# Performance work log

Measured on AMD Instinct MI355X. Metric: run time of the kernel, lower is better.

The kernel has to match this reference:

```python
import jax, jax.numpy as jnp
import numpy as np

# Dims: T time steps (PoissonEncoder seq_length=50), batch B, input N_IN, hidden H, labels L
T, B, N_IN, H, L = 50, 1024, 784, 256, 10
DT = 0.001            # norse default dt
TAU_SYN_INV = 100.0   # 1/0.01
TAU_MEM_INV = 50.0    # 1/0.02
V_LEAK, V_TH, V_RESET = 0.0, 0.5, 0.0
ALPHA = 100.0         # SuperSpike surrogate slope

@jax.custom_vjp
def superspike(x):
    # Heaviside forward, SuperSpike surrogate backward (norse 'super' method)
    return (x > 0).astype(x.dtype)

def _ss_fwd(x):
    return superspike(x), x

def _ss_bwd(x, g):
    return (g / (ALPHA * jnp.abs(x) + 1.0) ** 2,)

superspike.defvjp(_ss_fwd, _ss_bwd)

def setup_inputs() -> dict:
    key = jax.random.key(0)
    ks = jax.random.split(key, 5)
    # Poisson-encoded spike train, time-major [T, B, N_IN]
    x = (jax.random.uniform(ks[0], (T, B, N_IN)) < 0.3).astype(jnp.float32)
    Wi = jax.random.normal(ks[1], (H, N_IN), dtype=jnp.float32) / np.float32(np.sqrt(N_IN))
    Wr = jax.random.normal(ks[2], (H, H), dtype=jnp.float32) / np.float32(np.sqrt(H))
    Wout = jax.random.normal(ks[3], (L, H), dtype=jnp.float32) / np.float32(np.sqrt(H))
    bout = jnp.zeros((L,), dtype=jnp.float32)
    return {"x": x, "Wi": Wi, "Wr": Wr, "Wout": Wout, "bout": bout}

def reference(x, Wi, Wr, Wout, bout):
    Tw, Bb, _ = x.shape
    Hh = Wi.shape[0]
    Ll = Wout.shape[0]
    z0 = jnp.zeros((Bb, Hh), x.dtype)
    acc0 = jnp.zeros((Bb, Ll), x.dtype)

    def step(carry, x_t):
        z, v, i, acc = carry
        # LIF dynamics (norse lif_step)
        v_dec = v + DT * TAU_MEM_INV * ((V_LEAK - v) + i)   # voltage integration
        i_dec = i * (1.0 - DT * TAU_SYN_INV)                # synaptic current decay
        z_new = superspike(v_dec - V_TH)                    # spike
        v_new = (1.0 - z_new) * v_dec + z_new * V_RESET     # reset
        i_new = i_dec + x_t @ Wi.T + z @ Wr.T               # input + recurrent drive
        # per-step readout accumulation
        acc = acc + z_new @ Wout.T + bout
        return (z_new, v_new, i_new, acc), None

    (_, _, _, acc), _ = jax.lax.scan(step, (z0, z0, z0, acc0), x)
    return acc / Tw  # outputs.float() / time_window (is_test=False path)
```

## Files before the change

kernel.cpp:

```cpp
#include <hip/hip_runtime.h>
#include <cstdint>
#include <cstddef>

#define T_STEPS 50
#define B_SZ    1024
#define N_INP   784
#define H_SZ    256
#define L_SZ    10
#define M_TOT   (T_STEPS * B_SZ)
#define NK0     26
#define NSLICE  5

typedef int v4i  __attribute__((ext_vector_type(4)));
typedef int v16i __attribute__((ext_vector_type(16)));

__global__ __launch_bounds__(256) void transpose_wr(const float* __restrict__ Wr,
                                                    float* __restrict__ WrTz) {
    __shared__ float tile[32][33];
    int bx = blockIdx.x * 32, by = blockIdx.y * 32;
    int tx = threadIdx.x % 32, ty = threadIdx.x / 32;
    #pragma unroll
    for (int j = 0; j < 32; j += 8)
        tile[ty + j][tx] = Wr[(size_t)(by + ty + j) * H_SZ + bx + tx];
    __syncthreads();
    #pragma unroll
    for (int j = 0; j < 32; j += 8)
        WrTz[(size_t)(bx + ty + j) * H_SZ + by + tx] = tile[tx][ty + j];
}

__global__ __launch_bounds__(128) void prep_packed(const float* __restrict__ Wi,
                                                   uint8_t* __restrict__ SBp) {
    const int nt   = blockIdx.x;
    const int k0   = blockIdx.y * 2 + (threadIdx.x >> 6);
    const int lane = threadIdx.x & 63;
    const int h    = nt * 32 + (lane & 31);
    const int g    = k0 * 2 + (lane >> 5);

    int wd[NSLICE][4] = {};
    #pragma unroll
    for (int u = 0; u < 16; ++u) {
        double wv = 0.0;
        if (g < 49) wv = (double)Wi[(size_t)h * N_INP + g * 16 + u];
        double r = rint(wv * 0x1p40);
        #pragma unroll
        for (int j = 0; j < NSLICE - 1; ++j) {
            double q  = floor((r + 128.0) * 0.00390625);
            double dj = r - 256.0 * q;
            wd[j][u >> 2] |= ((int)dj & 0xFF) << ((u & 3) * 8);
            r = q;
        }
        wd[NSLICE - 1][u >> 2] |= ((int)r & 0xFF) << ((u & 3) * 8);
    }
    uint8_t* base = SBp + ((size_t)(nt * NK0 + k0) * NSLICE) * 1024 + lane * 16;
    #pragma unroll
    for (int j = 0; j < NSLICE; ++j)
        *(v4i*)(base + (size_t)j * 1024) = (v4i){wd[j][0], wd[j][1], wd[j][2], wd[j][3]};
}

__global__ __launch_bounds__(256) void pack_x(const float* __restrict__ X,
                                              uint8_t* __restrict__ Ap) {
    const int mt  = blockIdx.x;
    const int tid = threadIdx.x;
    #pragma unroll
    for (int i = 0; i < 7; ++i) {
        int s = tid + i * 256;
        if (s < NK0 * 64) {
            int k0 = s >> 6, lane = s & 63;
            int m = mt * 32 + (lane & 31);
            int g = k0 * 2 + (lane >> 5);
            unsigned int bw[4] = {0u, 0u, 0u, 0u};
            if (g < 49) {
                const float* src = X + (size_t)m * N_INP + g * 16;
                #pragma unroll
                for (int q = 0; q < 4; ++q) {
                    float4 f = *(const float4*)(src + q * 4);
                    bw[q] = (f.x != 0.f ? 1u : 0u) | (f.y != 0.f ? 0x100u : 0u)
                          | (f.z != 0.f ? 0x10000u : 0u) | (f.w != 0.f ? 0x1000000u : 0u);
                }
            }
            *(v4i*)(Ap + ((size_t)(mt * NK0 + k0)) * 1024 + lane * 16) =
                (v4i){(int)bw[0], (int)bw[1], (int)bw[2], (int)bw[3]};
        }
    }
}

__global__ __launch_bounds__(256) void gemm_i8s(const uint8_t* __restrict__ Ap,
                                                const uint8_t* __restrict__ SBp,
                                                double* __restrict__ cur) {
    __shared__ __align__(16) uint8_t Bs[2][2 * NSLICE * 1024];

    const int tid   = threadIdx.x;
    const int wave  = tid >> 6;
    const int lane  = tid & 63;
    const int ghalf = lane >> 5;
    const int nt    = blockIdx.y;
    const int mt0   = (blockIdx.x * 4 + wave) * 2;
    const int mt1   = mt0 + 1;

    const uint8_t* ap0 = Ap + (size_t)mt0 * NK0 * 1024 + lane * 16;
    const uint8_t* ap1 = Ap + (size_t)mt1 * NK0 * 1024 + lane * 16;
    const uint8_t* bbase = SBp + ((size_t)nt * NK0 * NSLICE) * 1024;

    {
        const uint8_t* src = bbase;
        #pragma unroll
        for (int i = 0; i < 2; ++i) {
            int s = tid + i * 256;
            *(v4i*)(Bs[0] + s * 16) = *(const v4i*)(src + s * 16);
        }
        if (tid < 128) {
            int s = tid + 512;
            *(v4i*)(Bs[0] + s * 16) = *(const v4i*)(src + s * 16);
        }
    }
    v4i a0c = *(const v4i*)(ap0);
    v4i a0n = *(const v4i*)(ap0 + 1024);
    v4i a1c = *(const v4i*)(ap1);
    v4i a1n = *(const v4i*)(ap1 + 1024);
    __syncthreads();

    v16i acc0[NSLICE] = {};
    v16i acc1[NSLICE] = {};

    for (int p = 0; p < 13; ++p) {
        const int cb = p & 1;
        v4i b0c = a0c, b0n = a0n, b1c = a1c, b1n = a1n;
        if (p < 12) {
            const uint8_t* src = bbase + (size_t)(p + 1) * 2 * NSLICE * 1024;
            uint8_t* dst = Bs[cb ^ 1];
            #pragma unroll
            for (int i = 0; i < 2; ++i) {
                int s = tid + i * 256;
                *(v4i*)(dst + s * 16) = *(const v4i*)(src + s * 16);
            }
            if (tid < 128) {
                int s = tid + 512;
                *(v4i*)(dst + s * 16) = *(const v4i*)(src + s * 16);
            }
            a0c = *(const v4i*)(ap0 + (size_t)(2 * p + 2) * 1024);
            a0n = *(const v4i*)(ap0 + (size_t)(2 * p + 3) * 1024);
            a1c = *(const v4i*)(ap1 + (size_t)(2 * p + 2) * 1024);
            a1n = *(const v4i*)(ap1 + (size_t)(2 * p + 3) * 1024);
        }
        #pragma unroll
        for (int dk = 0; dk < 2; ++dk) {
            v4i aa0 = dk ? b0n : b0c;
            v4i aa1 = dk ? b1n : b1c;
            #pragma unroll
            for (int j = 0; j < NSLICE; ++j) {
                v4i b = *(const v4i*)(Bs[cb] + (dk * NSLICE + j) * 1024 + lane * 16);
                acc0[j] = __builtin_amdgcn_mfma_i32_32x32x32_i8(aa0, b, acc0[j], 0, 0, 0);
                acc1[j] = __builtin_amdgcn_mfma_i32_32x32x32_i8(aa1, b, acc1[j], 0, 0, 0);
            }
        }
        __syncthreads();
    }

    const int h = nt * 32 + (lane & 31);
    #pragma unroll
    for (int r = 0; r < 16; ++r) {
        int mloc = (r & 3) + 8 * (r >> 2) + 4 * ghalf;
        double s0 = (double)acc0[4][r];
        s0 = s0 * 256.0 + (double)acc0[3][r];
        s0 = s0 * 256.0 + (double)acc0[2][r];
        s0 = s0 * 256.0 + (double)acc0[1][r];
        s0 = s0 * 256.0 + (double)acc0[0][r];
        cur[(size_t)(mt0 * 32 + mloc) * H_SZ + h] = s0 * 0x1p-40;
        double s1 = (double)acc1[4][r];
        s1 = s1 * 256.0 + (double)acc1[3][r];
        s1 = s1 * 256.0 + (double)acc1[2][r];
        s1 = s1 * 256.0 + (double)acc1[1][r];
        s1 = s1 * 256.0 + (double)acc1[0][r];
        cur[(size_t)(mt1 * 32 + mloc) * H_SZ + h] = s1 * 0x1p-40;
    }
}

__device__ __forceinline__ int build_list_pad(const unsigned long long* zm, int h,
                                              int* list) {
    unsigned long long w0 = zm[0], w1 = zm[1], w2 = zm[2], w3 = zm[3];
    int c0 = __popcll(w0), c1 = __popcll(w1), c2 = __popcll(w2), c3 = __popcll(w3);
    int wi = h >> 6;
    unsigned long long word = zm[wi];
    int base = (wi > 0 ? c0 : 0) + (wi > 1 ? c1 : 0) + (wi > 2 ? c2 : 0);
    int bit = h & 63;
    bool act = (word >> bit) & 1ull;
    int pos = __popcll(word & ((1ull << bit) - 1ull));
    if (act) list[base + pos] = h;
    int tot = c0 + c1 + c2 + c3;
    if (h < 8) list[tot + h] = 256;
    return tot;
}

__global__ __launch_bounds__(256) void snn_scan(const double* __restrict__ cur,
                                                const float* __restrict__ WrTz,
                                                const float* __restrict__ Wout,
                                                const float* __restrict__ bout,
                                                float* __restrict__ out) {
    const int b = blockIdx.x;
    const int h = threadIdx.x;

    __shared__ unsigned long long zmS[4];
    __shared__ int listS[2][H_SZ + 8];
    __shared__ float cntS[H_SZ];

    double v = 0.0, syn = 0.0;
    int cnt = 0;
    int nn[2] = {0, 0};

    const double* curb = cur + (size_t)b * H_SZ + h;
    const float*  wrh  = WrTz + h;
    double inp_c = curb[0];

    for (int t = 0; t < T_STEPS; ++t) {
        const int p = t & 1;
        int tn = (t < T_STEPS - 1) ? t + 1 : t;
        double inp_n = curb[(size_t)tn * B_SZ * H_SZ];

        double v_dec = v + 0.05 * ((0.0 - v) + syn);
        double i_dec = 0.9 * syn;
        bool   z_new = v_dec > 0.5;
        v = z_new ? 0.0 : v_dec;
        cnt += z_new ? 1 : 0;

        double r0 = 0.0, r1 = 0.0, r2 = 0.0, r3 = 0.0;
        const int* lp = listS[p];
        const int  n  = nn[p];
        for (int j = 0; j < n; j += 8) {
            float f0 = wrh[(size_t)lp[j + 0] * H_SZ];
            float f1 = wrh[(size_t)lp[j + 1] * H_SZ];
            float f2 = wrh[(size_t)lp[j + 2] * H_SZ];
            float f3 = wrh[(size_t)lp[j + 3] * H_SZ];
            float f4 = wrh[(size_t)lp[j + 4] * H_SZ];
            float f5 = wrh[(size_t)lp[j + 5] * H_SZ];
            float f6 = wrh[(size_t)lp[j + 6] * H_SZ];
            float f7 = wrh[(size_t)lp[j + 7] * H_SZ];
            r0 += (double)f0 + (double)f1;
            r1 += (double)f2 + (double)f3;
            r2 += (double)f4 + (double)f5;
            r3 += (double)f6 + (double)f7;
        }

        unsigned long long bal = __ballot((int)z_new);
        if ((h & 63) == 0) zmS[h >> 6] = bal;
        __syncthreads();
        nn[p ^ 1] = build_list_pad(zmS, h, listS[p ^ 1]);
        syn = (i_dec + inp_c) + ((r0 + r1) + (r2 + r3));
        inp_c = inp_n;
        __syncthreads();
    }

    cntS[h] = (float)cnt;
    __syncthreads();
    if (h < L_SZ) {
        double s = 0.0;
        for (int k = 0; k < H_SZ; ++k)
            s += (double)cntS[k] * (double)Wout[(size_t)h * H_SZ + k];
        s += (double)T_STEPS * (double)bout[h];
        out[(size_t)b * L_SZ + h] = (float)(s / (double)T_STEPS);
    }
}

extern "C" void kernel_launch(void* const* d_in, const int* in_sizes, int n_in,
                              void* d_out, int out_size, void* d_ws, size_t ws_size,
                              hipStream_t stream) {
    const float* x    = (const float*)d_in[0];
    const float* Wi   = (const float*)d_in[1];
    const float* Wr   = (const float*)d_in[2];
    const float* Wout = (const float*)d_in[3];
    const float* bout = (const float*)d_in[4];
    float* out = (float*)d_out;

    char* ws = (char*)d_ws;
    double*  cur  = (double*)(ws);
    float*   WrTz = (float*)(ws + 104857600);
    uint8_t* SBp  = (uint8_t*)(ws + 105121792);
    uint8_t* Ap   = (uint8_t*)(ws + 106186752);

    hipMemsetAsync(WrTz + 256 * H_SZ, 0, H_SZ * sizeof(float), stream);
    hipLaunchKernelGGL(transpose_wr, dim3(8, 8), dim3(256), 0, stream, Wr, WrTz);
    hipLaunchKernelGGL(prep_packed, dim3(8, 13), dim3(128), 0, stream, Wi, SBp);
    hipLaunchKernelGGL(pack_x, dim3(M_TOT / 32), dim3(256), 0, stream, x, Ap);
    hipLaunchKernelGGL(gemm_i8s, dim3(M_TOT / 256, 8), dim3(256), 0, stream, Ap, SBp, cur);
    hipLaunchKernelGGL(snn_scan, dim3(B_SZ), dim3(256), 0, stream,
                       cur, WrTz, Wout, bout, out);
}
```

Before: 405.4 us.

## Give each wavefront its own spike list and drop the second barrier in the SNN scan

```diff
diff --git a/kernel.cpp b/kernel.cpp
--- a/kernel.cpp
+++ b/kernel.cpp
@@ -22,6 +22,8 @@
     #pragma unroll
     for (int j = 0; j < 32; j += 8)
         tile[ty + j][tx] = Wr[(size_t)(by + ty + j) * H_SZ + bx + tx];
+    if (blockIdx.x == 0 && blockIdx.y == 0)
+        WrTz[(size_t)256 * H_SZ + threadIdx.x] = 0.0f;
     __syncthreads();
     #pragma unroll
     for (int j = 0; j < 32; j += 8)
@@ -175,32 +177,18 @@
     }
 }
 
-__device__ __forceinline__ int build_list_pad(const unsigned long long* zm, int h,
-                                              int* list) {
-    unsigned long long w0 = zm[0], w1 = zm[1], w2 = zm[2], w3 = zm[3];
-    int c0 = __popcll(w0), c1 = __popcll(w1), c2 = __popcll(w2), c3 = __popcll(w3);
-    int wi = h >> 6;
-    unsigned long long word = zm[wi];
-    int base = (wi > 0 ? c0 : 0) + (wi > 1 ? c1 : 0) + (wi > 2 ? c2 : 0);
-    int bit = h & 63;
-    bool act = (word >> bit) & 1ull;
-    int pos = __popcll(word & ((1ull << bit) - 1ull));
-    if (act) list[base + pos] = h;
-    int tot = c0 + c1 + c2 + c3;
-    if (h < 8) list[tot + h] = 256;
-    return tot;
-}
-
 __global__ __launch_bounds__(256) void snn_scan(const double* __restrict__ cur,
                                                 const float* __restrict__ WrTz,
                                                 const float* __restrict__ Wout,
                                                 const float* __restrict__ bout,
                                                 float* __restrict__ out) {
-    const int b = blockIdx.x;
-    const int h = threadIdx.x;
-
-    __shared__ unsigned long long zmS[4];
-    __shared__ int listS[2][H_SZ + 8];
+    const int b    = blockIdx.x;
+    const int h    = threadIdx.x;
+    const int wv   = h >> 6;
+    const int lane = h & 63;
+
+    __shared__ unsigned long long zmS[2][4];
+    __shared__ __align__(16) int listS[2][4][264];
     __shared__ float cntS[H_SZ];
 
     double v = 0.0, syn = 0.0;
@@ -208,11 +196,13 @@
     int nn[2] = {0, 0};
 
     const double* curb = cur + (size_t)b * H_SZ + h;
-    const float*  wrh  = WrTz + h;
+    const char*   wrb  = (const char*)WrTz;
+    const uint32_t hoff = (uint32_t)(h * 4);
     double inp_c = curb[0];
 
     for (int t = 0; t < T_STEPS; ++t) {
         const int p = t & 1;
+        const int q = p ^ 1;
         int tn = (t < T_STEPS - 1) ? t + 1 : t;
         double inp_n = curb[(size_t)tn * B_SZ * H_SZ];
 
@@ -223,17 +213,19 @@
         cnt += z_new ? 1 : 0;
 
         double r0 = 0.0, r1 = 0.0, r2 = 0.0, r3 = 0.0;
-        const int* lp = listS[p];
+        const int* lp = listS[p][wv];
         const int  n  = nn[p];
         for (int j = 0; j < n; j += 8) {
-            float f0 = wrh[(size_t)lp[j + 0] * H_SZ];
-            float f1 = wrh[(size_t)lp[j + 1] * H_SZ];
-            float f2 = wrh[(size_t)lp[j + 2] * H_SZ];
-            float f3 = wrh[(size_t)lp[j + 3] * H_SZ];
-            float f4 = wrh[(size_t)lp[j + 4] * H_SZ];
-            float f5 = wrh[(size_t)lp[j + 5] * H_SZ];
-            float f6 = wrh[(size_t)lp[j + 6] * H_SZ];
-            float f7 = wrh[(size_t)lp[j + 7] * H_SZ];
+            v4i w0 = *(const v4i*)(lp + j);
+            v4i w1 = *(const v4i*)(lp + j + 4);
+            float f0 = *(const float*)(wrb + ((uint32_t)w0.x + hoff));
+            float f1 = *(const float*)(wrb + ((uint32_t)w0.y + hoff));
+            float f2 = *(const float*)(wrb + ((uint32_t)w0.z + hoff));
+            float f3 = *(const float*)(wrb + ((uint32_t)w0.w + hoff));
+            float f4 = *(const float*)(wrb + ((uint32_t)w1.x + hoff));
+            float f5 = *(const float*)(wrb + ((uint32_t)w1.y + hoff));
+            float f6 = *(const float*)(wrb + ((uint32_t)w1.z + hoff));
+            float f7 = *(const float*)(wrb + ((uint32_t)w1.w + hoff));
             r0 += (double)f0 + (double)f1;
             r1 += (double)f2 + (double)f3;
             r2 += (double)f4 + (double)f5;
@@ -241,12 +233,33 @@
         }
 
         unsigned long long bal = __ballot((int)z_new);
-        if ((h & 63) == 0) zmS[h >> 6] = bal;
+        if (lane == 0) zmS[q][wv] = bal;
         __syncthreads();
-        nn[p ^ 1] = build_list_pad(zmS, h, listS[p ^ 1]);
+
+        {
+            unsigned long long m0 = zmS[q][0], m1 = zmS[q][1],
+                               m2 = zmS[q][2], m3 = zmS[q][3];
+            int c0 = __popcll(m0), c1 = __popcll(m1),
+                c2 = __popcll(m2), c3 = __popcll(m3);
+            const int wi = lane >> 4;
+            unsigned long long word = zmS[q][wi];
+            int basew = (wi > 0 ? c0 : 0) + (wi > 1 ? c1 : 0) + (wi > 2 ? c2 : 0);
+            int* lw = listS[q][wv];
+            const int hb = 4 * lane;
+            #pragma unroll
+            for (int u = 0; u < 4; ++u) {
+                int bit = (hb + u) & 63;
+                bool act = (word >> bit) & 1ull;
+                int  pos = __popcll(word & ((1ull << bit) - 1ull));
+                if (act) lw[basew + pos] = (hb + u) << 10;
+            }
+            int tot = c0 + c1 + c2 + c3;
+            if (lane < 8) lw[tot + lane] = 256 << 10;
+            nn[q] = tot;
+        }
+
         syn = (i_dec + inp_c) + ((r0 + r1) + (r2 + r3));
         inp_c = inp_n;
-        __syncthreads();
     }
 
     cntS[h] = (float)cnt;
@@ -276,7 +289,6 @@
     uint8_t* SBp  = (uint8_t*)(ws + 105121792);
     uint8_t* Ap   = (uint8_t*)(ws + 106186752);
 
-    hipMemsetAsync(WrTz + 256 * H_SZ, 0, H_SZ * sizeof(float), stream);
     hipLaunchKernelGGL(transpose_wr, dim3(8, 8), dim3(256), 0, stream, Wr, WrTz);
     hipLaunchKernelGGL(prep_packed, dim3(8, 13), dim3(128), 0, stream, Wi, SBp);
     hipLaunchKernelGGL(pack_x, dim3(M_TOT / 32), dim3(256), 0, stream, x, Ap);
```

Result: faster. 396.5 us (-2.2%).

## Pack four batches per scan block and stage half of Wr in LDS

Applied to the files above, without the earlier changes.

```diff
diff --git a/kernel.cpp b/kernel.cpp
--- a/kernel.cpp
+++ b/kernel.cpp
@@ -22,6 +22,8 @@
     #pragma unroll
     for (int j = 0; j < 32; j += 8)
         tile[ty + j][tx] = Wr[(size_t)(by + ty + j) * H_SZ + bx + tx];
+    if (blockIdx.x == 0 && blockIdx.y == 0)
+        WrTz[(size_t)256 * H_SZ + threadIdx.x] = 0.0f;
     __syncthreads();
     #pragma unroll
     for (int j = 0; j < 32; j += 8)
@@ -175,86 +177,137 @@
     }
 }
 
-__device__ __forceinline__ int build_list_pad(const unsigned long long* zm, int h,
-                                              int* list) {
-    unsigned long long w0 = zm[0], w1 = zm[1], w2 = zm[2], w3 = zm[3];
-    int c0 = __popcll(w0), c1 = __popcll(w1), c2 = __popcll(w2), c3 = __popcll(w3);
-    int wi = h >> 6;
-    unsigned long long word = zm[wi];
-    int base = (wi > 0 ? c0 : 0) + (wi > 1 ? c1 : 0) + (wi > 2 ? c2 : 0);
-    int bit = h & 63;
-    bool act = (word >> bit) & 1ull;
-    int pos = __popcll(word & ((1ull << bit) - 1ull));
-    if (act) list[base + pos] = h;
-    int tot = c0 + c1 + c2 + c3;
-    if (h < 8) list[tot + h] = 256;
-    return tot;
-}
-
-__global__ __launch_bounds__(256) void snn_scan(const double* __restrict__ cur,
-                                                const float* __restrict__ WrTz,
-                                                const float* __restrict__ Wout,
-                                                const float* __restrict__ bout,
-                                                float* __restrict__ out) {
-    const int b = blockIdx.x;
-    const int h = threadIdx.x;
-
-    __shared__ unsigned long long zmS[4];
-    __shared__ int listS[2][H_SZ + 8];
-    __shared__ float cntS[H_SZ];
+#define SNN_STEP(T_CUR, P_, Q_, nnLp, nnGp, nnLq, nnGq)                           \
+  {                                                                               \
+                                          \
+    double v_dec = v + 0.05 * ((0.0 - v) + syn);                                  \
+    double i_dec = 0.9 * syn;                                                     \
+    bool   z_new = v_dec > 0.5;                                                   \
+    v = z_new ? 0.0 : v_dec;                                                      \
+    cnt += z_new ? 1 : 0;                                                         \
+    unsigned long long bal = __ballot((int)z_new);                                \
+    if (lane == 0) zmS[Q_][bl][wv] = bal;                                         \
+    __syncthreads();                               \
+          \
+    int tn = ((T_CUR) < T_STEPS - 1) ? (T_CUR) + 1 : (T_CUR);                     \
+    double inp_n = curb[(size_t)tn * (B_SZ * H_SZ)];                              \
+                      \
+    {                                                                             \
+      unsigned long long m0 = zmS[Q_][bl][0], m1 = zmS[Q_][bl][1],                \
+                         m2 = zmS[Q_][bl][2], m3 = zmS[Q_][bl][3];                \
+      int c0 = __popcll(m0), c1 = __popcll(m1);                                   \
+      int c2 = __popcll(m2), c3 = __popcll(m3);                                   \
+      int cL = c0 + c1, cG = c2 + c3;                                             \
+      unsigned long long word = (h < 64) ? m0 : (h < 128) ? m1                    \
+                               : (h < 192) ? m2 : m3;                             \
+      int bit = h & 63;                                                           \
+      bool act = (word >> bit) & 1ull;                                            \
+      int pos = __popcll(word & ((1ull << bit) - 1ull));                          \
+      if (h < 128) {                                                              \
+        if (act) listL[Q_][bl][((h >> 6) ? c0 : 0) + pos] = h << 8;               \
+        if (h < 16) listL[Q_][bl][cL + h] = 128 << 8;           \
+      } else {                                                                    \
+        if (act) listG[Q_][bl][(((h >> 6) == 3) ? c2 : 0) + pos] = h << 10;       \
+        if (h < 144) listG[Q_][bl][cG + (h - 128)] = 256 << 10;    \
+      }                                                                           \
+      nnLq = cL; nnGq = cG;                                                       \
+    }                                                                             \
+        \
+    double r0 = 0.0, r1 = 0.0, r2 = 0.0, r3 = 0.0;                                \
+    const int nG = nnGp, nL = nnLp;                                               \
+    const int* lg = &listG[P_][bl][0];                                            \
+    const int* ll = &listL[P_][bl][0];                                            \
+    float g0, g1, g2, g3, g4, g5, g6, g7;                                         \
+    if (nG > 0) {                                        \
+      v4i w0 = *(const v4i*)(lg);                                                 \
+      v4i w1 = *(const v4i*)(lg + 4);                                             \
+      g0 = *(const float*)(wrb + ((uint32_t)w0.x + hoff));                        \
+      g1 = *(const float*)(wrb + ((uint32_t)w0.y + hoff));                        \
+      g2 = *(const float*)(wrb + ((uint32_t)w0.z + hoff));                        \
+      g3 = *(const float*)(wrb + ((uint32_t)w0.w + hoff));                        \
+      g4 = *(const float*)(wrb + ((uint32_t)w1.x + hoff));                        \
+      g5 = *(const float*)(wrb + ((uint32_t)w1.y + hoff));                        \
+      g6 = *(const float*)(wrb + ((uint32_t)w1.z + hoff));                        \
+      g7 = *(const float*)(wrb + ((uint32_t)w1.w + hoff));                        \
+    }                                                                             \
+    for (int j = 0; j < nL; j += 8) {                             \
+      v4i u0 = *(const v4i*)(ll + j);                                             \
+      v4i u1 = *(const v4i*)(ll + j + 4);                                         \
+      float e0 = wrlh[u0.x], e1 = wrlh[u0.y], e2 = wrlh[u0.z], e3 = wrlh[u0.w];   \
+      float e4 = wrlh[u1.x], e5 = wrlh[u1.y], e6 = wrlh[u1.z], e7 = wrlh[u1.w];   \
+      r0 += (double)e0 + (double)e1;                                              \
+      r1 += (double)e2 + (double)e3;                                              \
+      r2 += (double)e4 + (double)e5;                                              \
+      r3 += (double)e6 + (double)e7;                                              \
+    }                                                                             \
+    for (int j = 0; j < nG; j += 8) {               \
+      float c0f = g0, c1f = g1, c2f = g2, c3f = g3;                               \
+      float c4f = g4, c5f = g5, c6f = g6, c7f = g7;                               \
+      v4i w0 = *(const v4i*)(lg + j + 8);                \
+      v4i w1 = *(const v4i*)(lg + j + 12);                                        \
+      g0 = *(const float*)(wrb + ((uint32_t)w0.x + hoff));                        \
+      g1 = *(const float*)(wrb + ((uint32_t)w0.y + hoff));                        \
+      g2 = *(const float*)(wrb + ((uint32_t)w0.z + hoff));                        \
+      g3 = *(const float*)(wrb + ((uint32_t)w0.w + hoff));                        \
+      g4 = *(const float*)(wrb + ((uint32_t)w1.x + hoff));                        \
+      g5 = *(const float*)(wrb + ((uint32_t)w1.y + hoff));                        \
+      g6 = *(const float*)(wrb + ((uint32_t)w1.z + hoff));                        \
+      g7 = *(const float*)(wrb + ((uint32_t)w1.w + hoff));                        \
+      r0 += (double)c0f + (double)c1f;                                            \
+      r1 += (double)c2f + (double)c3f;                                            \
+      r2 += (double)c4f + (double)c5f;                                            \
+      r3 += (double)c6f + (double)c7f;                                            \
+    }                                                                             \
+    syn = (i_dec + inp_c) + ((r0 + r1) + (r2 + r3));                              \
+    inp_c = inp_n;                                                                \
+  }
+
+__global__ __launch_bounds__(1024) void snn_scan(const double* __restrict__ cur,
+                                                 const float* __restrict__ WrTz,
+                                                 const float* __restrict__ Wout,
+                                                 const float* __restrict__ bout,
+                                                 float* __restrict__ out) {
+    const int tid  = threadIdx.x;
+    const int bl   = tid >> 8;
+    const int h    = tid & 255;
+    const int lane = tid & 63;
+    const int wv   = (tid >> 6) & 3;
+    const int b    = blockIdx.x * 4 + bl;
+
+    __shared__ __align__(16) float WrL[129 * 256];
+    __shared__ unsigned long long zmS[2][4][4];
+    __shared__ __align__(16) int listL[2][4][144];
+    __shared__ __align__(16) int listG[2][4][144];
+    __shared__ float cntS[4][256];
+
+    for (int s = tid; s < (129 * 256) / 4; s += 1024) {
+        float4 val = (s < 8192) ? ((const float4*)WrTz)[s]
+                                : make_float4(0.f, 0.f, 0.f, 0.f);
+        ((float4*)WrL)[s] = val;
+    }
+    __syncthreads();
 
     double v = 0.0, syn = 0.0;
     int cnt = 0;
-    int nn[2] = {0, 0};
-
-    const double* curb = cur + (size_t)b * H_SZ + h;
-    const float*  wrh  = WrTz + h;
+    int nnL0 = 0, nnG0 = 0, nnL1 = 0, nnG1 = 0;
+
+    const double*  curb = cur + (size_t)b * H_SZ + h;
+    const char*    wrb  = (const char*)WrTz;
+    const float*   wrlh = WrL + h;
+    const uint32_t hoff = (uint32_t)(h * 4);
     double inp_c = curb[0];
 
-    for (int t = 0; t < T_STEPS; ++t) {
-        const int p = t & 1;
-        int tn = (t < T_STEPS - 1) ? t + 1 : t;
-        double inp_n = curb[(size_t)tn * B_SZ * H_SZ];
-
-        double v_dec = v + 0.05 * ((0.0 - v) + syn);
-        double i_dec = 0.9 * syn;
-        bool   z_new = v_dec > 0.5;
-        v = z_new ? 0.0 : v_dec;
-        cnt += z_new ? 1 : 0;
-
-        double r0 = 0.0, r1 = 0.0, r2 = 0.0, r3 = 0.0;
-        const int* lp = listS[p];
-        const int  n  = nn[p];
-        for (int j = 0; j < n; j += 8) {
-            float f0 = wrh[(size_t)lp[j + 0] * H_SZ];
-            float f1 = wrh[(size_t)lp[j + 1] * H_SZ];
-            float f2 = wrh[(size_t)lp[j + 2] * H_SZ];
-            float f3 = wrh[(size_t)lp[j + 3] * H_SZ];
-            float f4 = wrh[(size_t)lp[j + 4] * H_SZ];
-            float f5 = wrh[(size_t)lp[j + 5] * H_SZ];
-            float f6 = wrh[(size_t)lp[j + 6] * H_SZ];
-            float f7 = wrh[(size_t)lp[j + 7] * H_SZ];
-            r0 += (double)f0 + (double)f1;
-            r1 += (double)f2 + (double)f3;
-            r2 += (double)f4 + (double)f5;
-            r3 += (double)f6 + (double)f7;
-        }
-
-        unsigned long long bal = __ballot((int)z_new);
-        if ((h & 63) == 0) zmS[h >> 6] = bal;
-        __syncthreads();
-        nn[p ^ 1] = build_list_pad(zmS, h, listS[p ^ 1]);
-        syn = (i_dec + inp_c) + ((r0 + r1) + (r2 + r3));
-        inp_c = inp_n;
-        __syncthreads();
-    }
-
-    cntS[h] = (float)cnt;
+    for (int t2 = 0; t2 < T_STEPS; t2 += 2) {
+        SNN_STEP(t2,     0, 1, nnL0, nnG0, nnL1, nnG1);
+        SNN_STEP(t2 + 1, 1, 0, nnL1, nnG1, nnL0, nnG0);
+    }
+
+    cntS[bl][h] = (float)cnt;
     __syncthreads();
     if (h < L_SZ) {
         double s = 0.0;
         for (int k = 0; k < H_SZ; ++k)
-            s += (double)cntS[k] * (double)Wout[(size_t)h * H_SZ + k];
+            s += (double)cntS[bl][k] * (double)Wout[(size_t)h * H_SZ + k];
         s += (double)T_STEPS * (double)bout[h];
         out[(size_t)b * L_SZ + h] = (float)(s / (double)T_STEPS);
     }
@@ -276,11 +329,10 @@
     uint8_t* SBp  = (uint8_t*)(ws + 105121792);
     uint8_t* Ap   = (uint8_t*)(ws + 106186752);
 
-    hipMemsetAsync(WrTz + 256 * H_SZ, 0, H_SZ * sizeof(float), stream);
     hipLaunchKernelGGL(transpose_wr, dim3(8, 8), dim3(256), 0, stream, Wr, WrTz);
     hipLaunchKernelGGL(prep_packed, dim3(8, 13), dim3(128), 0, stream, Wi, SBp);
     hipLaunchKernelGGL(pack_x, dim3(M_TOT / 32), dim3(256), 0, stream, x, Ap);
     hipLaunchKernelGGL(gemm_i8s, dim3(M_TOT / 256, 8), dim3(256), 0, stream, Ap, SBp, cur);
-    hipLaunchKernelGGL(snn_scan, dim3(B_SZ), dim3(256), 0, stream,
+    hipLaunchKernelGGL(snn_scan, dim3(B_SZ / 4), dim3(1024), 0, stream,
                        cur, WrTz, Wout, bout, out);
 }
```

Measured after the change: 401.4 us. About the same (-1.0%).
